# Performance work log

Measured on AMD Instinct MI355X. Metric: run time of the kernel, lower is better.

## Reference

```python
import jax, jax.numpy as jnp
import numpy as np

B, S, D, H = 2, 2048, 2048, 16
DH = D // H  # 128
ROPE_BASE = 10000.0


def setup_inputs() -> dict:
    key = jax.random.key(0)
    ks = jax.random.split(key, 5)
    scale = 0.02
    return {
        "x": jax.random.normal(ks[0], (B, S, D), dtype=jnp.float32),
        "wq": jax.random.normal(ks[1], (D, D), dtype=jnp.float32) * scale,
        "wk": jax.random.normal(ks[2], (D, D), dtype=jnp.float32) * scale,
        "wv": jax.random.normal(ks[3], (D, D), dtype=jnp.float32) * scale,
        "wo": jax.random.normal(ks[4], (D, D), dtype=jnp.float32) * scale,
    }


def _rope_cache(seq_len, dhead):
    # flash-attn RotaryEmbedding: inv_freq over even dims, full rotary_dim = dhead
    inv_freq = 1.0 / (ROPE_BASE ** (jnp.arange(0, dhead, 2, dtype=jnp.float32) / dhead))
    t = jnp.arange(seq_len, dtype=jnp.float32)
    freqs = jnp.einsum("s,d->sd", t, inv_freq)  # [S, DH/2]
    return jnp.cos(freqs), jnp.sin(freqs)


def _apply_rope_interleaved(t, cos, sin):
    # t: [B, S, H, DH]; interleaved pairs (t[...,0::2], t[...,1::2])
    te, to = t[..., 0::2], t[..., 1::2]
    c = cos[None, :, None, :]
    s = sin[None, :, None, :]
    re = te * c - to * s
    ro = te * s + to * c
    return jnp.stack([re, ro], axis=-1).reshape(t.shape)


def reference(x, wq, wk, wv, wo):
    b, s, d = x.shape
    q = (x @ wq).reshape(b, s, H, DH)
    k = (x @ wk).reshape(b, s, H, DH)
    v = (x @ wv).reshape(b, s, H, DH)

    cos, sin = _rope_cache(s, DH)
    q = _apply_rope_interleaved(q.astype(jnp.float32), cos, sin)
    k = _apply_rope_interleaved(k.astype(jnp.float32), cos, sin)

    # flash_attn_func(causal=True) semantics: bf16 inputs, fp32 softmax, scale 1/sqrt(dhead)
    qb = q.astype(jnp.bfloat16)
    kb = k.astype(jnp.bfloat16)
    vb = v.astype(jnp.bfloat16)
    scale = 1.0 / np.sqrt(DH)
    scores = jnp.einsum("bqhd,bkhd->bhqk", qb, kb,
                        preferred_element_type=jnp.float32) * scale
    causal = jnp.tril(jnp.ones((s, s), dtype=bool))
    scores = jnp.where(causal[None, None], scores, -jnp.inf)
    p = jax.nn.softmax(scores, axis=-1)  # fp32
    attn = jnp.einsum("bhqk,bkhd->bqhd", p.astype(jnp.bfloat16), vb,
                      preferred_element_type=jnp.float32)
    attn = attn.astype(jnp.bfloat16).astype(x.dtype)  # flash returns bf16, then .to(x)
    out = attn.reshape(b, s, d) @ wo
    return out
```

## Files before the change

### kernel.cpp

```cpp
#include <hip/hip_runtime.h>
#include <hip/hip_bf16.h>
#include <stdint.h>

#define B_SZ   2
#define S_LEN  2048
#define DMODEL 2048
#define NH     16
#define DHD    128

typedef __attribute__((ext_vector_type(8))) __bf16 bf16x8;
typedef __attribute__((ext_vector_type(4))) float  f32x4;
typedef __attribute__((ext_vector_type(4))) float  float4v;
typedef __attribute__((ext_vector_type(8))) unsigned short ushort8;
typedef __attribute__((ext_vector_type(4))) unsigned short ushort4v;

__device__ __forceinline__ unsigned short f2bf(float f) {
  unsigned int u = __float_as_uint(f);
  unsigned int r = (u + 0x7fffu + ((u >> 16) & 1u)) >> 16;
  return (unsigned short)r;
}

__device__ __forceinline__ unsigned int cvt_pk_bf16(float lo, float hi) {
  unsigned int r;
  asm("v_cvt_pk_bf16_f32 %0, %1, %2" : "=v"(r) : "v"(lo), "v"(hi));
  return r;
}

__device__ __forceinline__ void async_cp16(void* lds, const void* g) {
  __builtin_amdgcn_global_load_lds(
      (const __attribute__((address_space(1))) void*)g,
      (__attribute__((address_space(3))) void*)lds, 16, 0, 0);
}

__global__ __launch_bounds__(256) void k_cast_bf16(const float* __restrict__ in,
                                                   unsigned short* __restrict__ out,
                                                   int n4) {
  int i = blockIdx.x * 256 + threadIdx.x;
  if (i >= n4) return;
  float4v v = ((const float4v*)in)[i];
  ushort4v o;
  o[0] = f2bf(v[0]); o[1] = f2bf(v[1]); o[2] = f2bf(v[2]); o[3] = f2bf(v[3]);
  ((ushort4v*)out)[i] = o;
}

__global__ __launch_bounds__(256) void k_transpose_all(const float* __restrict__ w0,
                                                       const float* __restrict__ w1,
                                                       const float* __restrict__ w2,
                                                       const float* __restrict__ w3,
                                                       unsigned short* __restrict__ WTbase) {
  __shared__ unsigned short tile[64 * 72];
  const int z = blockIdx.z;
  const float* W = (z == 0) ? w0 : (z == 1) ? w1 : (z == 2) ? w2 : w3;
  unsigned short* WT = WTbase + (size_t)z * 4194304;
  const int n0 = blockIdx.x * 64;
  const int k0 = blockIdx.y * 64;
  const int t = threadIdx.x;
#pragma unroll
  for (int i = 0; i < 4; ++i) {
    int c = t + 256 * i;
    int r = c >> 4, c4 = c & 15;
    float4v v = *(const float4v*)(W + (size_t)(k0 + r) * DMODEL + n0 + c4 * 4);
    ushort4v o;
    o[0] = f2bf(v[0]); o[1] = f2bf(v[1]); o[2] = f2bf(v[2]); o[3] = f2bf(v[3]);
    *(ushort4v*)(&tile[r * 72 + c4 * 4]) = o;
  }
  __syncthreads();
#pragma unroll
  for (int i = 0; i < 2; ++i) {
    int c = t + 256 * i;
    int n = c >> 3, k8 = c & 7;
    ushort8 o;
#pragma unroll
    for (int j = 0; j < 8; ++j) o[j] = tile[(k8 * 8 + j) * 72 + n];
    *(ushort8*)(WT + (size_t)(n0 + n) * DMODEL + k0 + k8 * 8) = o;
  }
}

__global__ __launch_bounds__(256) void k_rope_table(float* __restrict__ cosT,
                                                    float* __restrict__ sinT) {
  int i = blockIdx.x * 256 + threadIdx.x;
  int s = i >> 6, dj = i & 63;
  float e = __expf(-9.210340371976184f * (float)dj * (1.0f / 64.0f));
  float f = (float)s * e;
  cosT[i] = cosf(f);
  sinT[i] = sinf(f);
}

template <int EPI>
__global__ __launch_bounds__(512, 2) void k_gemm128(
    const unsigned short* __restrict__ A,
    const unsigned short* __restrict__ BT,
    float* __restrict__ C0,
    unsigned short* __restrict__ Cq,
    unsigned short* __restrict__ Ck,
    unsigned short* __restrict__ Cv,
    const float* __restrict__ cosT,
    const float* __restrict__ sinT,
    int chn) {
  __shared__ char smem[98304];
  const int tid = threadIdx.x;

  const int xcd = blockIdx.x & 7;
  const int idx = blockIdx.x >> 3;
  const int bm = (xcd >> 2) * 16 + (idx & 15);
  const int bn = (xcd & 3) * chn + (idx >> 4);

  const int gs = (tid & 7) ^ ((tid >> 3) & 7);
  const unsigned short* Abase = A + (size_t)(bm * 128 + (tid >> 3)) * 2048 + gs * 8;
  const unsigned short* Bbase = BT + (size_t)(bn * 256 + (tid >> 3)) * 2048 + gs * 8;
  const int dstA = tid * 16;
  const int dstB = 16384 + tid * 16;

  const int lane = tid & 63, wid = tid >> 6;
  const int wr = wid >> 2, wcn = wid & 3;
  const int lr = lane & 15, hi = lane >> 4;
  int aoff[4][2], boff[4][2];
#pragma unroll
  for (int m = 0; m < 4; ++m) {
    int row = wr * 64 + m * 16 + lr;
#pragma unroll
    for (int k = 0; k < 2; ++k)
      aoff[m][k] = row * 128 + ((((k * 4 + hi)) ^ (row & 7)) << 4);
  }
#pragma unroll
  for (int n = 0; n < 4; ++n) {
    int row = wcn * 64 + n * 16 + lr;
#pragma unroll
    for (int k = 0; k < 2; ++k)
      boff[n][k] = 16384 + row * 128 + ((((k * 4 + hi)) ^ (row & 7)) << 4);
  }

  f32x4 acc[4][4];
#pragma unroll
  for (int m = 0; m < 4; ++m)
#pragma unroll
    for (int n = 0; n < 4; ++n) {
      f32x4 z = {0.f, 0.f, 0.f, 0.f};
      acc[m][n] = z;
    }

#define STG_A(c, t_) do {                                                   \
    const unsigned short* _s = Abase + (t_) * 64;                           \
    async_cp16(smem + (c) * 49152 + dstA, _s);                              \
    async_cp16(smem + (c) * 49152 + dstA + 8192, _s + 64 * 2048);           \
  } while (0)
#define STG_B(c, t_) do {                                                   \
    const unsigned short* _s = Bbase + (t_) * 64;                           \
    async_cp16(smem + (c) * 49152 + dstB, _s);                              \
    async_cp16(smem + (c) * 49152 + dstB + 8192, _s + 64 * 2048);           \
    async_cp16(smem + (c) * 49152 + dstB + 16384, _s + 128 * 2048);         \
    async_cp16(smem + (c) * 49152 + dstB + 24576, _s + 192 * 2048);         \
  } while (0)

  auto tile = [&](int T, int CC, bool DO_A, bool DO_B, int VM) __attribute__((always_inline)) {
    const char* Sb = smem + CC * 49152;
    bf16x8 a0[4], b0[4], a1[4], b1[4];
#pragma unroll
    for (int m = 0; m < 4; ++m) a0[m] = *(const bf16x8*)(Sb + aoff[m][0]);
#pragma unroll
    for (int n = 0; n < 4; ++n) b0[n] = *(const bf16x8*)(Sb + boff[n][0]);
    __builtin_amdgcn_sched_barrier(0);
#pragma unroll
    for (int m = 0; m < 4; ++m) a1[m] = *(const bf16x8*)(Sb + aoff[m][1]);
#pragma unroll
    for (int n = 0; n < 4; ++n) b1[n] = *(const bf16x8*)(Sb + boff[n][1]);
    if (DO_A) STG_A(CC ^ 1, T + 1);
    asm volatile("s_waitcnt lgkmcnt(8)" ::: "memory");
    __builtin_amdgcn_sched_barrier(0);
    __builtin_amdgcn_s_setprio(1);
#pragma unroll
    for (int m = 0; m < 4; ++m)
#pragma unroll
      for (int n = 0; n < 4; ++n)
        acc[m][n] = __builtin_amdgcn_mfma_f32_16x16x32_bf16(a0[m], b0[n], acc[m][n], 0, 0, 0);
    __builtin_amdgcn_s_setprio(0);
    __builtin_amdgcn_s_barrier();
    __builtin_amdgcn_sched_barrier(0);
    asm volatile("s_waitcnt lgkmcnt(0)" ::: "memory");
    __builtin_amdgcn_sched_barrier(0);
    if (DO_B) STG_B(CC, T + 2);
    __builtin_amdgcn_s_setprio(1);
#pragma unroll
    for (int m = 0; m < 4; ++m)
#pragma unroll
      for (int n = 0; n < 4; ++n)
        acc[m][n] = __builtin_amdgcn_mfma_f32_16x16x32_bf16(a1[m], b1[n], acc[m][n], 0, 0, 0);
    __builtin_amdgcn_s_setprio(0);
    if (VM == 0) asm volatile("s_waitcnt vmcnt(4)" ::: "memory");
    else if (VM == 1) asm volatile("s_waitcnt vmcnt(0)" ::: "memory");
    if (VM != 2) {
      __builtin_amdgcn_s_barrier();
      __builtin_amdgcn_sched_barrier(0);
    }
  };

  STG_B(0, 0);
  STG_A(0, 0);
  STG_B(1, 1);
  asm volatile("s_waitcnt vmcnt(4)" ::: "memory");
  __builtin_amdgcn_s_barrier();
  __builtin_amdgcn_sched_barrier(0);

  for (int it = 0; it < 15; ++it) {
    tile(2 * it, 0, true, true, 0);
    tile(2 * it + 1, 1, true, true, 0);
  }
  tile(30, 0, true, false, 1);
  tile(31, 1, false, false, 2);

  const int row_b = bm * 128 + wr * 64 + hi * 4;
  const int col_b = bn * 256 + wcn * 64 + lr;
  if (EPI == 0) {
#pragma unroll
    for (int m = 0; m < 4; ++m)
#pragma unroll
      for (int n = 0; n < 4; ++n) {
        int col = col_b + n * 16;
#pragma unroll
        for (int j = 0; j < 4; ++j) {
          int row = row_b + m * 16 + j;
          C0[(size_t)row * 2048 + col] = acc[m][n][j];
        }
      }
  } else {
    const int sel = bn >> 3;
#pragma unroll
    for (int m = 0; m < 4; ++m) {
#pragma unroll
      for (int n = 0; n < 4; ++n) {
        int col = col_b + n * 16;
        int hh = (col >> 7) & 15, d = col & 127;
        if (sel == 2) {
#pragma unroll
          for (int j = 0; j < 4; ++j) {
            int row = row_b + m * 16 + j;
            int b = row >> 11, s = row & 2047;
            Cv[((size_t)(b * NH + hh) * S_LEN + s) * DHD + d] = f2bf(acc[m][n][j]);
          }
        } else {
          unsigned short* dst = sel ? Ck : Cq;
          int dj = d >> 1;
          float sgn = (d & 1) ? 1.f : -1.f;
#pragma unroll
          for (int j = 0; j < 4; ++j) {
            int row = row_b + m * 16 + j;
            int b = row >> 11, s = row & 2047;
            float v = acc[m][n][j];
            float pp = __shfl_xor(v, 1);
            float cc = cosT[(s << 6) + dj];
            float sn = sinT[(s << 6) + dj];
            dst[((size_t)(b * NH + hh) * S_LEN + s) * DHD + d] = f2bf(v * cc + sgn * pp * sn);
          }
        }
      }
    }
  }
#undef STG_A
#undef STG_B
}

__global__ __launch_bounds__(256) void k_flash_attn(const unsigned short* __restrict__ Qg,
                                                    const unsigned short* __restrict__ Kg,
                                                    const unsigned short* __restrict__ Vg,
                                                    unsigned short* __restrict__ Og) {
  __shared__ unsigned short K_lds[2][64 * 128];
  __shared__ unsigned short VT_lds[2][128 * 64];

  const int pq = blockIdx.x, h = blockIdx.y, b = blockIdx.z;
  const int t = threadIdx.x;
  const int lane = t & 63, wave = t >> 6;
  const int hi = lane >> 4, lr = lane & 15;

  const size_t head = (size_t)(b * NH + h) * (size_t)(S_LEN * DHD);
  const unsigned short* Q = Qg + head;
  const unsigned short* Kp = Kg + head;
  const unsigned short* Vp = Vg + head;

  const int kr0 = t >> 4;
  const int kgc = (t & 15) ^ (kr0 & 7);
  const unsigned short* Kbase = Kp + (size_t)kr0 * DHD + kgc * 8;
  const int kdst = t * 16;

  const int vdc = t & 15, vsp0 = t >> 4;
  const unsigned short* Vbase = Vp + (size_t)(2 * vsp0) * DHD + vdc * 8;
  const int bo0 = 16 * ((vsp0 >> 1) & 3) + 8 * ((vsp0 >> 3) & 1) + 4 * (vsp0 & 1);

  const float sc = 0.08838834764831845f;

  for (int pass = 0; pass < 2; ++pass) {
    const int qt = (pass == 0) ? pq : (31 - pq);
    const int nt = qt + 1;
    const int qbase = qt * 64 + wave * 16;
    const int qrow = qbase + lr;

    bf16x8 qf[4];
    {
      const unsigned short* qr_ = Q + (size_t)(qbase + lr) * DHD;
#pragma unroll
      for (int kc = 0; kc < 4; ++kc) qf[kc] = *(const bf16x8*)(qr_ + kc * 32 + hi * 8);
    }

    f32x4 of[8];
#pragma unroll
    for (int i = 0; i < 8; ++i) {
      f32x4 z = {0.f, 0.f, 0.f, 0.f};
      of[i] = z;
    }
    float mS = -INFINITY;
    float lsum = 0.f;

    {
#pragma unroll
      for (int i = 0; i < 4; ++i)
        async_cp16((char*)K_lds[0] + kdst + i * 4096, Kbase + (size_t)(16 * i) * DHD);
      ushort8 va0 = *(const ushort8*)(Vbase);
      ushort8 vb0 = *(const ushort8*)(Vbase + DHD);
      ushort8 va1 = *(const ushort8*)(Vbase + (size_t)32 * DHD);
      ushort8 vb1 = *(const ushort8*)(Vbase + (size_t)33 * DHD);
#pragma unroll
      for (int j = 0; j < 8; ++j) {
        int row = vdc * 8 + j;
        int swz = ((j ^ vdc) & 7) << 4;
        *(unsigned int*)((char*)VT_lds[0] + row * 128 + (bo0 ^ swz)) =
            (unsigned int)va0[j] | ((unsigned int)vb0[j] << 16);
        *(unsigned int*)((char*)VT_lds[0] + row * 128 + ((bo0 | 64) ^ swz)) =
            (unsigned int)va1[j] | ((unsigned int)vb1[j] << 16);
      }
    }
    __syncthreads();

    for (int tt = 0; tt < nt; ++tt) {
      const int cur = tt & 1;
      const int kv0 = tt * 64;
      const bool more = (tt + 1 < nt);
      const bool diag = (tt == qt);

      ushort8 va0, vb0, va1, vb1;
      if (more) {
        const unsigned short* ks = Kbase + (size_t)(kv0 + 64) * DHD;
#pragma unroll
        for (int i = 0; i < 4; ++i)
          async_cp16((char*)K_lds[cur ^ 1] + kdst + i * 4096, ks + (size_t)(16 * i) * DHD);
        const unsigned short* vs = Vbase + (size_t)(kv0 + 64) * DHD;
        va0 = *(const ushort8*)(vs);
        vb0 = *(const ushort8*)(vs + DHD);
        va1 = *(const ushort8*)(vs + (size_t)32 * DHD);
        vb1 = *(const ushort8*)(vs + (size_t)33 * DHD);
      }

      const char* Kb = (const char*)K_lds[cur];
      f32x4 sf[4];
#pragma unroll
      for (int n = 0; n < 4; ++n) {
        f32x4 z = {0.f, 0.f, 0.f, 0.f};
        sf[n] = z;
      }
      __builtin_amdgcn_s_setprio(1);
#pragma unroll
      for (int n = 0; n < 4; ++n) {
        const int kr = n * 16 + lr;
        const int kswz = (kr & 7) << 4;
#pragma unroll
        for (int kc = 0; kc < 4; ++kc) {
          bf16x8 kf = *(const bf16x8*)(Kb + kr * 256 + ((kc * 64 + hi * 16) ^ kswz));
          sf[n] = __builtin_amdgcn_mfma_f32_16x16x32_bf16(kf, qf[kc], sf[n], 0, 0, 0);
        }
      }
      __builtin_amdgcn_s_setprio(0);

      float p[4][4];
      float mx = -INFINITY;
      if (diag) {
#pragma unroll
        for (int n = 0; n < 4; ++n)
#pragma unroll
          for (int j = 0; j < 4; ++j) {
            int kvcol = kv0 + n * 16 + hi * 4 + j;
            float v = (kvcol > qrow) ? -INFINITY : sf[n][j];
            p[n][j] = v;
            mx = fmaxf(mx, v);
          }
      } else {
#pragma unroll
        for (int n = 0; n < 4; ++n)
#pragma unroll
          for (int j = 0; j < 4; ++j) {
            float v = sf[n][j];
            p[n][j] = v;
            mx = fmaxf(mx, v);
          }
      }
      mx = fmaxf(mx, __shfl_xor(mx, 16));
      mx = fmaxf(mx, __shfl_xor(mx, 32));
      float mn = fmaxf(mS, mx);
      float corr = __expf((mS - mn) * sc);
      mS = mn;
      float mns = mn * sc;
      float rs = 0.f;
#pragma unroll
      for (int n = 0; n < 4; ++n)
#pragma unroll
        for (int j = 0; j < 4; ++j) {
          float e = __expf(__builtin_fmaf(p[n][j], sc, -mns));
          p[n][j] = e;
          rs += e;
        }
      rs += __shfl_xor(rs, 16);
      rs += __shfl_xor(rs, 32);
      lsum = lsum * corr + rs;

      unsigned int pk[4][2];
#pragma unroll
      for (int n = 0; n < 4; ++n) {
        pk[n][0] = cvt_pk_bf16(p[n][0], p[n][1]);
        pk[n][1] = cvt_pk_bf16(p[n][2], p[n][3]);
      }

      float corrb[4];
#pragma unroll
      for (int j = 0; j < 4; ++j) corrb[j] = __shfl(corr, hi * 4 + j);
#pragma unroll
      for (int nd = 0; nd < 8; ++nd)
#pragma unroll
        for (int j = 0; j < 4; ++j) of[nd][j] *= corrb[j];

      const char* Vb = (const char*)VT_lds[cur];
      __builtin_amdgcn_s_setprio(1);
#pragma unroll
      for (int kc = 0; kc < 2; ++kc) {
        union { unsigned int u[4]; bf16x8 v; } pa;
        pa.u[0] = pk[2 * kc][0];
        pa.u[1] = pk[2 * kc][1];
        pa.u[2] = pk[2 * kc + 1][0];
        pa.u[3] = pk[2 * kc + 1][1];
#pragma unroll
        for (int nd = 0; nd < 8; ++nd) {
          const int vr = nd * 16 + lr;
          const int vswz = ((vr & 7) ^ ((vr >> 3) & 7)) << 4;
          bf16x8 vf = *(const bf16x8*)(Vb + vr * 128 + ((kc * 64 + hi * 16) ^ vswz));
          of[nd] = __builtin_amdgcn_mfma_f32_16x16x32_bf16(pa.v, vf, of[nd], 0, 0, 0);
        }
      }
      __builtin_amdgcn_s_setprio(0);

      if (more) {
        char* Vw = (char*)VT_lds[cur ^ 1];
#pragma unroll
        for (int j = 0; j < 8; ++j) {
          int row = vdc * 8 + j;
          int swz = ((j ^ vdc) & 7) << 4;
          *(unsigned int*)(Vw + row * 128 + (bo0 ^ swz)) =
              (unsigned int)va0[j] | ((unsigned int)vb0[j] << 16);
          *(unsigned int*)(Vw + row * 128 + ((bo0 | 64) ^ swz)) =
              (unsigned int)va1[j] | ((unsigned int)vb1[j] << 16);
        }
      }
      __syncthreads();
    }

    float inv[4];
#pragma unroll
    for (int j = 0; j < 4; ++j) {
      float ls = __shfl(lsum, hi * 4 + j);
      inv[j] = 1.0f / ls;
    }
#pragma unroll
    for (int nd = 0; nd < 8; ++nd)
#pragma unroll
      for (int j = 0; j < 4; ++j) {
        int qr = qbase + hi * 4 + j;
        Og[((size_t)(b * S_LEN + qr) * NH + h) * DHD + nd * 16 + lr] = f2bf(of[nd][j] * inv[j]);
      }
  }
}

extern "C" void kernel_launch(void* const* d_in, const int* in_sizes, int n_in,
                              void* d_out, int out_size, void* d_ws, size_t ws_size,
                              hipStream_t stream) {
  const float* x  = (const float*)d_in[0];
  const float* wq = (const float*)d_in[1];
  const float* wk = (const float*)d_in[2];
  const float* wv = (const float*)d_in[3];
  const float* wo = (const float*)d_in[4];
  float* out = (float*)d_out;

  char* ws = (char*)d_ws;
  unsigned short* xb    = (unsigned short*)(ws);
  unsigned short* wqT   = (unsigned short*)(ws + 16777216);
  unsigned short* woT   = (unsigned short*)(ws + 41943040);
  unsigned short* qb    = (unsigned short*)(ws + 50331648);
  unsigned short* kb    = (unsigned short*)(ws + 67108864);
  unsigned short* vb    = (unsigned short*)(ws + 83886080);
  float*          cosT  = (float*)(ws + 100663296);
  float*          sinT  = (float*)(ws + 101187584);
  unsigned short* attnb = xb;

  k_cast_bf16<<<8192, 256, 0, stream>>>(x, xb, 2097152);
  dim3 tg(32, 32, 4);
  k_transpose_all<<<tg, 256, 0, stream>>>(wq, wk, wv, wo, wqT);
  k_rope_table<<<512, 256, 0, stream>>>(cosT, sinT);

  k_gemm128<1><<<768, 512, 0, stream>>>(xb, wqT, nullptr, qb, kb, vb, cosT, sinT, 6);

  dim3 ga(16, 16, 2);
  k_flash_attn<<<ga, 256, 0, stream>>>(qb, kb, vb, attnb);

  k_gemm128<0><<<256, 512, 0, stream>>>(attnb, woT, out, nullptr, nullptr, nullptr,
                                        nullptr, nullptr, 2);
}
```

Before: 240.5 us.

## Process two query sub-tiles per wave in flash attention; reschedule GEMM LDS loads

The flash-attention kernel now gives each block a 128-row query tile: every wave keeps two 16-row query sets with separate softmax state. Each K/V tile loaded into LDS therefore feeds twice the MFMA work, and the grid is halved. Causal masking is tracked per sub-tile, and sub-tiles that lie entirely above the diagonal are skipped with zero probabilities. The GEMM inner tile is also rescheduled so the second-half LDS fragment loads sit between two halves of the first MFMA batch, with a full lgkmcnt wait. The cost is higher register pressure and fewer blocks for load balancing.

```diff
diff --git a/kernel.cpp b/kernel.cpp
--- a/kernel.cpp
+++ b/kernel.cpp
@@ -159,20 +159,28 @@
     for (int m = 0; m < 4; ++m) a0[m] = *(const bf16x8*)(Sb + aoff[m][0]);
 #pragma unroll
     for (int n = 0; n < 4; ++n) b0[n] = *(const bf16x8*)(Sb + boff[n][0]);
-    __builtin_amdgcn_sched_barrier(0);
-#pragma unroll
-    for (int m = 0; m < 4; ++m) a1[m] = *(const bf16x8*)(Sb + aoff[m][1]);
-#pragma unroll
-    for (int n = 0; n < 4; ++n) b1[n] = *(const bf16x8*)(Sb + boff[n][1]);
     if (DO_A) STG_A(CC ^ 1, T + 1);
-    asm volatile("s_waitcnt lgkmcnt(8)" ::: "memory");
+    asm volatile("s_waitcnt lgkmcnt(0)" ::: "memory");
     __builtin_amdgcn_sched_barrier(0);
     __builtin_amdgcn_s_setprio(1);
 #pragma unroll
-    for (int m = 0; m < 4; ++m)
-#pragma unroll
-      for (int n = 0; n < 4; ++n)
-        acc[m][n] = __builtin_amdgcn_mfma_f32_16x16x32_bf16(a0[m], b0[n], acc[m][n], 0, 0, 0);
+    for (int m = 0; m < 4; ++m) {
+      acc[m][0] = __builtin_amdgcn_mfma_f32_16x16x32_bf16(a0[m], b0[0], acc[m][0], 0, 0, 0);
+      acc[m][1] = __builtin_amdgcn_mfma_f32_16x16x32_bf16(a0[m], b0[1], acc[m][1], 0, 0, 0);
+    }
+    __builtin_amdgcn_s_setprio(0);
+    __builtin_amdgcn_sched_barrier(0);
+#pragma unroll
+    for (int m = 0; m < 4; ++m) a1[m] = *(const bf16x8*)(Sb + aoff[m][1]);
+#pragma unroll
+    for (int n = 0; n < 4; ++n) b1[n] = *(const bf16x8*)(Sb + boff[n][1]);
+    __builtin_amdgcn_sched_barrier(0);
+    __builtin_amdgcn_s_setprio(1);
+#pragma unroll
+    for (int m = 0; m < 4; ++m) {
+      acc[m][2] = __builtin_amdgcn_mfma_f32_16x16x32_bf16(a0[m], b0[2], acc[m][2], 0, 0, 0);
+      acc[m][3] = __builtin_amdgcn_mfma_f32_16x16x32_bf16(a0[m], b0[3], acc[m][3], 0, 0, 0);
+    }
     __builtin_amdgcn_s_setprio(0);
     __builtin_amdgcn_s_barrier();
     __builtin_amdgcn_sched_barrier(0);
@@ -288,26 +296,31 @@
   const float sc = 0.08838834764831845f;
 
   for (int pass = 0; pass < 2; ++pass) {
-    const int qt = (pass == 0) ? pq : (31 - pq);
-    const int nt = qt + 1;
-    const int qbase = qt * 64 + wave * 16;
-    const int qrow = qbase + lr;
-
-    bf16x8 qf[4];
+    const int qt = (pass == 0) ? pq : (15 - pq);
+    const int nt = 2 * (qt + 1);
+    const int qb0 = qt * 128 + wave * 16;
+    const int qb1 = qb0 + 64;
+
+    bf16x8 qf0[4], qf1[4];
     {
-      const unsigned short* qr_ = Q + (size_t)(qbase + lr) * DHD;
-#pragma unroll
-      for (int kc = 0; kc < 4; ++kc) qf[kc] = *(const bf16x8*)(qr_ + kc * 32 + hi * 8);
-    }
-
-    f32x4 of[8];
+      const unsigned short* qr0 = Q + (size_t)(qb0 + lr) * DHD;
+      const unsigned short* qr1 = Q + (size_t)(qb1 + lr) * DHD;
+#pragma unroll
+      for (int kc = 0; kc < 4; ++kc) {
+        qf0[kc] = *(const bf16x8*)(qr0 + kc * 32 + hi * 8);
+        qf1[kc] = *(const bf16x8*)(qr1 + kc * 32 + hi * 8);
+      }
+    }
+
+    f32x4 of0[8], of1[8];
 #pragma unroll
     for (int i = 0; i < 8; ++i) {
       f32x4 z = {0.f, 0.f, 0.f, 0.f};
-      of[i] = z;
-    }
-    float mS = -INFINITY;
-    float lsum = 0.f;
+      of0[i] = z;
+      of1[i] = z;
+    }
+    float mS0 = -INFINITY, mS1 = -INFINITY;
+    float ls0 = 0.f, ls1 = 0.f;
 
     {
 #pragma unroll
@@ -333,7 +346,6 @@
       const int cur = tt & 1;
       const int kv0 = tt * 64;
       const bool more = (tt + 1 < nt);
-      const bool diag = (tt == qt);
 
       ushort8 va0, vb0, va1, vb1;
       if (more) {
@@ -349,11 +361,12 @@
       }
 
       const char* Kb = (const char*)K_lds[cur];
-      f32x4 sf[4];
+      f32x4 sf0[4], sf1[4];
 #pragma unroll
       for (int n = 0; n < 4; ++n) {
         f32x4 z = {0.f, 0.f, 0.f, 0.f};
-        sf[n] = z;
+        sf0[n] = z;
+        sf1[n] = z;
       }
       __builtin_amdgcn_s_setprio(1);
 #pragma unroll
@@ -363,82 +376,103 @@
 #pragma unroll
         for (int kc = 0; kc < 4; ++kc) {
           bf16x8 kf = *(const bf16x8*)(Kb + kr * 256 + ((kc * 64 + hi * 16) ^ kswz));
-          sf[n] = __builtin_amdgcn_mfma_f32_16x16x32_bf16(kf, qf[kc], sf[n], 0, 0, 0);
+          sf0[n] = __builtin_amdgcn_mfma_f32_16x16x32_bf16(kf, qf0[kc], sf0[n], 0, 0, 0);
+          sf1[n] = __builtin_amdgcn_mfma_f32_16x16x32_bf16(kf, qf1[kc], sf1[n], 0, 0, 0);
         }
       }
       __builtin_amdgcn_s_setprio(0);
 
-      float p[4][4];
-      float mx = -INFINITY;
-      if (diag) {
-#pragma unroll
-        for (int n = 0; n < 4; ++n)
-#pragma unroll
-          for (int j = 0; j < 4; ++j) {
-            int kvcol = kv0 + n * 16 + hi * 4 + j;
-            float v = (kvcol > qrow) ? -INFINITY : sf[n][j];
-            p[n][j] = v;
-            mx = fmaxf(mx, v);
-          }
-      } else {
-#pragma unroll
-        for (int n = 0; n < 4; ++n)
-#pragma unroll
-          for (int j = 0; j < 4; ++j) {
-            float v = sf[n][j];
-            p[n][j] = v;
-            mx = fmaxf(mx, v);
-          }
-      }
-      mx = fmaxf(mx, __shfl_xor(mx, 16));
-      mx = fmaxf(mx, __shfl_xor(mx, 32));
-      float mn = fmaxf(mS, mx);
-      float corr = __expf((mS - mn) * sc);
-      mS = mn;
-      float mns = mn * sc;
-      float rs = 0.f;
-#pragma unroll
-      for (int n = 0; n < 4; ++n)
+      unsigned int pk0[4][2], pk1[4][2];
+      float cb0[4], cb1[4];
+      const bool act0 = kv0 <= qb0 + 15;
+      const bool act1 = kv0 <= qb1 + 15;
+
+#define SOFTMAX_SET(SF, MS, LS, PK, CB, QB, ACT) do {                        \
+    if (ACT) {                                                               \
+      float p_[4][4];                                                        \
+      float mx = -INFINITY;                                                  \
+      const int qrow_ = (QB) + lr;                                           \
+      if (kv0 + 63 > (QB)) {                                                 \
+        _Pragma("unroll")                                                    \
+        for (int n = 0; n < 4; ++n)                                          \
+          _Pragma("unroll")                                                  \
+          for (int j = 0; j < 4; ++j) {                                      \
+            int kvcol = kv0 + n * 16 + hi * 4 + j;                           \
+            float v = (kvcol > qrow_) ? -INFINITY : SF[n][j];                \
+            p_[n][j] = v;                                                    \
+            mx = fmaxf(mx, v);                                               \
+          }                                                                  \
+      } else {                                                               \
+        _Pragma("unroll")                                                    \
+        for (int n = 0; n < 4; ++n)                                          \
+          _Pragma("unroll")                                                  \
+          for (int j = 0; j < 4; ++j) {                                      \
+            float v = SF[n][j];                                              \
+            p_[n][j] = v;                                                    \
+            mx = fmaxf(mx, v);                                               \
+          }                                                                  \
+      }                                                                      \
+      mx = fmaxf(mx, __shfl_xor(mx, 16));                                    \
+      mx = fmaxf(mx, __shfl_xor(mx, 32));                                    \
+      float mn = fmaxf(MS, mx);                                              \
+      float corr = __expf((MS - mn) * sc);                                   \
+      MS = mn;                                                               \
+      float mns = mn * sc;                                                   \
+      float rs = 0.f;                                                        \
+      _Pragma("unroll")                                                      \
+      for (int n = 0; n < 4; ++n)                                            \
+        _Pragma("unroll")                                                    \
+        for (int j = 0; j < 4; ++j) {                                        \
+          float e = __expf(__builtin_fmaf(p_[n][j], sc, -mns));              \
+          p_[n][j] = e;                                                      \
+          rs += e;                                                           \
+        }                                                                    \
+      rs += __shfl_xor(rs, 16);                                              \
+      rs += __shfl_xor(rs, 32);                                              \
+      LS = LS * corr + rs;                                                   \
+      _Pragma("unroll")                                                      \
+      for (int n = 0; n < 4; ++n) {                                          \
+        PK[n][0] = cvt_pk_bf16(p_[n][0], p_[n][1]);                          \
+        PK[n][1] = cvt_pk_bf16(p_[n][2], p_[n][3]);                          \
+      }                                                                      \
+      _Pragma("unroll")                                                      \
+      for (int j = 0; j < 4; ++j) CB[j] = __shfl(corr, hi * 4 + j);          \
+    } else {                                                                 \
+      _Pragma("unroll")                                                      \
+      for (int n = 0; n < 4; ++n) { PK[n][0] = 0u; PK[n][1] = 0u; }          \
+      _Pragma("unroll")                                                      \
+      for (int j = 0; j < 4; ++j) CB[j] = 1.f;                               \
+    }                                                                        \
+  } while (0)
+
+      SOFTMAX_SET(sf0, mS0, ls0, pk0, cb0, qb0, act0);
+      SOFTMAX_SET(sf1, mS1, ls1, pk1, cb1, qb1, act1);
+#undef SOFTMAX_SET
+
+#pragma unroll
+      for (int nd = 0; nd < 8; ++nd)
 #pragma unroll
         for (int j = 0; j < 4; ++j) {
-          float e = __expf(__builtin_fmaf(p[n][j], sc, -mns));
-          p[n][j] = e;
-          rs += e;
+          of0[nd][j] *= cb0[j];
+          of1[nd][j] *= cb1[j];
         }
-      rs += __shfl_xor(rs, 16);
-      rs += __shfl_xor(rs, 32);
-      lsum = lsum * corr + rs;
-
-      unsigned int pk[4][2];
-#pragma unroll
-      for (int n = 0; n < 4; ++n) {
-        pk[n][0] = cvt_pk_bf16(p[n][0], p[n][1]);
-        pk[n][1] = cvt_pk_bf16(p[n][2], p[n][3]);
-      }
-
-      float corrb[4];
-#pragma unroll
-      for (int j = 0; j < 4; ++j) corrb[j] = __shfl(corr, hi * 4 + j);
-#pragma unroll
-      for (int nd = 0; nd < 8; ++nd)
-#pragma unroll
-        for (int j = 0; j < 4; ++j) of[nd][j] *= corrb[j];
 
       const char* Vb = (const char*)VT_lds[cur];
       __builtin_amdgcn_s_setprio(1);
 #pragma unroll
       for (int kc = 0; kc < 2; ++kc) {
-        union { unsigned int u[4]; bf16x8 v; } pa;
-        pa.u[0] = pk[2 * kc][0];
-        pa.u[1] = pk[2 * kc][1];
-        pa.u[2] = pk[2 * kc + 1][0];
-        pa.u[3] = pk[2 * kc + 1][1];
+        union { unsigned int u[4]; bf16x8 v; } pa0, pa1;
+        pa0.u[0] = pk0[2 * kc][0];     pa0.u[1] = pk0[2 * kc][1];
+        pa0.u[2] = pk0[2 * kc + 1][0]; pa0.u[3] = pk0[2 * kc + 1][1];
+        pa1.u[0] = pk1[2 * kc][0];     pa1.u[1] = pk1[2 * kc][1];
+        pa1.u[2] = pk1[2 * kc + 1][0]; pa1.u[3] = pk1[2 * kc + 1][1];
 #pragma unroll
         for (int nd = 0; nd < 8; ++nd) {
           const int vr = nd * 16 + lr;
           const int vswz = ((vr & 7) ^ ((vr >> 3) & 7)) << 4;
           bf16x8 vf = *(const bf16x8*)(Vb + vr * 128 + ((kc * 64 + hi * 16) ^ vswz));
-          of[nd] = __builtin_amdgcn_mfma_f32_16x16x32_bf16(pa.v, vf, of[nd], 0, 0, 0);
+          of0[nd] = __builtin_amdgcn_mfma_f32_16x16x32_bf16(pa0.v, vf, of0[nd], 0, 0, 0);
+          of1[nd] = __builtin_amdgcn_mfma_f32_16x16x32_bf16(pa1.v, vf, of1[nd], 0, 0, 0);
         }
       }
       __builtin_amdgcn_s_setprio(0);
@@ -458,18 +492,20 @@
       __syncthreads();
     }
 
-    float inv[4];
+    float inv0[4], inv1[4];
 #pragma unroll
     for (int j = 0; j < 4; ++j) {
-      float ls = __shfl(lsum, hi * 4 + j);
-      inv[j] = 1.0f / ls;
+      inv0[j] = 1.0f / __shfl(ls0, hi * 4 + j);
+      inv1[j] = 1.0f / __shfl(ls1, hi * 4 + j);
     }
 #pragma unroll
     for (int nd = 0; nd < 8; ++nd)
 #pragma unroll
       for (int j = 0; j < 4; ++j) {
-        int qr = qbase + hi * 4 + j;
-        Og[((size_t)(b * S_LEN + qr) * NH + h) * DHD + nd * 16 + lr] = f2bf(of[nd][j] * inv[j]);
+        int qr0 = qb0 + hi * 4 + j;
+        int qr1 = qb1 + hi * 4 + j;
+        Og[((size_t)(b * S_LEN + qr0) * NH + h) * DHD + nd * 16 + lr] = f2bf(of0[nd][j] * inv0[j]);
+        Og[((size_t)(b * S_LEN + qr1) * NH + h) * DHD + nd * 16 + lr] = f2bf(of1[nd][j] * inv1[j]);
       }
   }
 }
@@ -502,7 +538,7 @@
 
   k_gemm128<1><<<768, 512, 0, stream>>>(xb, wqT, nullptr, qb, kb, vb, cosT, sinT, 6);
 
-  dim3 ga(16, 16, 2);
+  dim3 ga(8, 16, 2);
   k_flash_attn<<<ga, 256, 0, stream>>>(qb, kb, vb, attnb);
 
   k_gemm128<0><<<256, 512, 0, stream>>>(attnb, woT, out, nullptr, nullptr, nullptr,
```

After: 258.1 us. +7.3%, slower.
